# Optimization experiments

Measured on AMD Instinct MI355X. Metric: run time of the kernel, lower is better.

Reference implementation:

```python
import jax, jax.numpy as jnp
import numpy as np

TEMPERATURE = 0.2

def setup_inputs() -> dict:
    key = jax.random.key(0)
    k1, k2 = jax.random.split(key)
    projected = jax.random.normal(k1, (2048, 2, 256), dtype=jnp.float32)
    predicted = jax.random.normal(k2, (2048, 4, 256), dtype=jnp.float32)
    return {"projected": projected, "predicted": predicted}

def _l2norm(x, eps=1e-12):
    n = jnp.linalg.norm(x, axis=-1, keepdims=True)
    return x / jnp.maximum(n, eps)

def reference(projected, predicted):
    # projected: [B, Vg, D], predicted: [B, Vt, D], Vt >= Vg.
    # Single-process: all_gather is identity, rank=0 -> labels = arange(B).
    B, Vg, D = projected.shape
    Vt = predicted.shape[1]
    Vl = Vt - Vg
    p = _l2norm(projected)
    q = _l2norm(predicted)
    # All pairwise similarity matrices at once: [Vg, Vt, B, B]
    logits = jnp.einsum('bid,cjd->ijbc', p, q) / TEMPERATURE
    lse = jax.nn.logsumexpr if False else jax.scipy.special.logsumexp(logits, axis=-1)  # [Vg, Vt, B]
    diag = jnp.diagonal(logits, axis1=-2, axis2=-1)                                    # [Vg, Vt, B]
    L = jnp.mean(lse - diag, axis=-1)  # per-pair CE loss, shape [Vg, Vt]
    # global terms: i != ii, both in [0, Vg)
    global_sum = jnp.sum(L[:, :Vg] * (1.0 - jnp.eye(Vg, dtype=L.dtype)))
    num_global_terms = Vg * (Vg - 1)
    global_loss = global_sum / num_global_terms if num_global_terms > 0 else jnp.float32(0.0)
    # local terms: faithful to source -> predicted columns 0..Vl-1 (not offset)
    num_local_terms = Vg * Vl
    local_sum = jnp.sum(L[:, :Vl]) if Vl > 0 else jnp.float32(0.0)
    local_loss = local_sum / num_local_terms if num_local_terms > 0 else jnp.float32(0.0)
    num_terms = num_global_terms + num_local_terms
    total = (global_sum + local_sum) / num_terms
    return (total, global_loss, local_loss)
```

## Files before the change

kernel.cpp:

```cpp
#include <hip/hip_runtime.h>
#include <hip/hip_bf16.h>
#include <hip/hip_fp8.h>
#include <stdint.h>

#define TB 2048
#define TD 256

typedef long long                                         fp8x8;
typedef __attribute__((ext_vector_type(8)))  int          int8v;
typedef __attribute__((ext_vector_type(16))) float        f32x16;

union frag32 { fp8x8 g[4]; int8v v; };

#define SQRT5 2.23606797749979f
#define SCALE1 0x7F

__global__ __launch_bounds__(256) void nnclr_prep(const float* __restrict__ proj,
                                                  const float* __restrict__ pred,
                                                  unsigned char* __restrict__ pq2) {
    const int grp = blockIdx.x;
    const int v   = blockIdx.y;
    const int t   = threadIdx.x;

    __shared__ float rowbuf[32][260];
    __shared__ float scales[32];

    #pragma unroll
    for (int it = 0; it < 8; ++it) {
        const int f = it * 256 + t;
        const int m = f >> 6, q = f & 63;
        const int b = grp * 32 + m;
        const float4* src = (v < 2) ? (const float4*)(proj + ((size_t)b * 2 + v) * TD)
                                    : (const float4*)(pred + ((size_t)b * 4 + (v - 2)) * TD);
        const float4 val = src[q];
        *(float4*)&rowbuf[m][q * 4] = val;
    }
    __syncthreads();

    {
        const int row = t >> 3, l8 = t & 7;
        float ss = 0.f;
        #pragma unroll
        for (int n = 0; n < 32; ++n) { const float y = rowbuf[row][l8 + 8 * n]; ss += y * y; }
        ss += __shfl_xor(ss, 1, 64);
        ss += __shfl_xor(ss, 2, 64);
        ss += __shfl_xor(ss, 4, 64);
        if (l8 == 0) scales[row] = SQRT5 / fmaxf(sqrtf(ss), 1e-12f);
    }
    __syncthreads();

    unsigned int* dst32 = (unsigned int*)(pq2 + (size_t)(v * 64 + grp) * 8192);
    #pragma unroll
    for (int it = 0; it < 8; ++it) {
        const int u   = it * 256 + t;
        const int m   = u >> 6;
        const int col = (u >> 1) & 31;
        const int e4  = u & 1;
        const float sc = scales[col];
        unsigned int w = 0;
        #pragma unroll
        for (int i = 0; i < 4; ++i) {
            const float y = rowbuf[col][m * 8 + 4 * e4 + i] * sc;
            const __hip_fp8_e4m3 f8(y);
            w |= ((unsigned int)f8.__x) << (8 * i);
        }
        dst32[u] = w;
    }
}

__global__ __launch_bounds__(256, 2) void nnclr_main(const unsigned char* __restrict__ pq2,
                                                     float* __restrict__ sPart,
                                                     float* __restrict__ dPart)
{
    const int rb = blockIdx.x, ch = blockIdx.y, j = blockIdx.z;
    const int tid = threadIdx.x, lane = tid & 63, wave = tid >> 6;
    const int cl = lane & 31, hk = lane >> 5;
    const int b0 = rb * 32;

    const fp8x8* P = (const fp8x8*)pq2;
    frag32 aF0[4], aF1[4];
    #pragma unroll
    for (int kb = 0; kb < 4; ++kb) {
        #pragma unroll
        for (int q = 0; q < 4; ++q) {
            const int g = 8 * kb + 4 * hk + q;
            aF0[kb].g[q] = P[((0 * 64 + rb) * 32 + g) * 32 + cl];
            aF1[kb].g[q] = P[((1 * 64 + rb) * 32 + g) * 32 + cl];
        }
    }

    float sAcc0[16], sAcc1[16];
    #pragma unroll
    for (int r = 0; r < 16; ++r) { sAcc0[r] = 0.f; sAcc1[r] = 0.f; }
    float d0 = 0.f, d1 = 0.f;
    const int  rDiag    = (cl & 3) + 4 * (cl >> 3);
    const bool laneDiag = (((cl >> 2) & 1) == hk);

    const fp8x8* Bbase = P + (size_t)(2 + j) * 64 * 32 * 32;
    const int cg0 = ch * 16 + wave * 4;

    frag32 bf[2][4];
    #pragma unroll
    for (int kb = 0; kb < 4; ++kb)
        #pragma unroll
        for (int q = 0; q < 4; ++q)
            bf[0][kb].g[q] = Bbase[((size_t)cg0 * 32 + 8 * kb + 4 * hk + q) * 32 + cl];

    #pragma unroll
    for (int cgl = 0; cgl < 4; ++cgl) {
        const int cg = cg0 + cgl;
        if (cgl < 3) {
            #pragma unroll
            for (int kb = 0; kb < 4; ++kb)
                #pragma unroll
                for (int q = 0; q < 4; ++q)
                    bf[(cgl + 1) & 1][kb].g[q] =
                        Bbase[((size_t)(cg + 1) * 32 + 8 * kb + 4 * hk + q) * 32 + cl];
        }
        f32x16 acc0, acc1;
        #pragma unroll
        for (int r = 0; r < 16; ++r) { acc0[r] = 0.f; acc1[r] = 0.f; }
        #pragma unroll
        for (int kb = 0; kb < 4; ++kb) {
            acc0 = __builtin_amdgcn_mfma_scale_f32_32x32x64_f8f6f4(
                       aF0[kb].v, bf[cgl & 1][kb].v, acc0, 0, 0, 0, SCALE1, 0, SCALE1);
            acc1 = __builtin_amdgcn_mfma_scale_f32_32x32x64_f8f6f4(
                       aF1[kb].v, bf[cgl & 1][kb].v, acc1, 0, 0, 0, SCALE1, 0, SCALE1);
        }
        const bool diagCG = (cg == rb);
        #pragma unroll
        for (int r = 0; r < 16; ++r) {
            const float v0 = acc0[r], v1 = acc1[r];
            sAcc0[r] += __expf(v0 - 5.0f);
            sAcc1[r] += __expf(v1 - 5.0f);
            if (diagCG) {
                const bool m = laneDiag && (r == rDiag);
                d0 += m ? v0 : 0.f;
                d1 += m ? v1 : 0.f;
            }
        }
    }

    #pragma unroll
    for (int r = 0; r < 16; ++r) {
        float s0 = sAcc0[r], s1 = sAcc1[r];
        #pragma unroll
        for (int msk = 1; msk < 32; msk <<= 1) {
            s0 += __shfl_xor(s0, msk, 64);
            s1 += __shfl_xor(s1, msk, 64);
        }
        sAcc0[r] = s0; sAcc1[r] = s1;
    }

    __shared__ float sArr[2][4][32];
    __shared__ float dArr[2][4][32];
    if (cl == 0) {
        #pragma unroll
        for (int r = 0; r < 16; ++r) {
            const int rowl = (r & 3) + 8 * (r >> 2) + 4 * hk;
            sArr[0][wave][rowl] = sAcc0[r];
            sArr[1][wave][rowl] = sAcc1[r];
        }
    }
    if (laneDiag) { dArr[0][wave][cl] = d0; dArr[1][wave][cl] = d1; }
    __syncthreads();
    if (tid < 64) {
        const int i = tid >> 5, row = tid & 31;
        float s = 0.f, d = 0.f;
        #pragma unroll
        for (int w = 0; w < 4; ++w) { s += sArr[i][w][row]; d += dArr[i][w][row]; }
        const int pair = i * 2 + j;
        const int b = b0 + row;
        sPart[((size_t)pair * TB + b) * 4 + ch] = s;
        dPart[((size_t)pair * TB + b) * 4 + ch] = d;
    }
}

__global__ __launch_bounds__(1024) void nnclr_final(const float* __restrict__ sPart,
                                                    const float* __restrict__ dPart,
                                                    float* __restrict__ out) {
    const int tid = threadIdx.x;
    float acc[4] = {0.f, 0.f, 0.f, 0.f};
    #pragma unroll
    for (int k = 0; k < 8; ++k) {
        const int item = k * 1024 + tid;
        const float4 sv = ((const float4*)sPart)[item];
        const float4 dv = ((const float4*)dPart)[item];
        const float s = (sv.x + sv.y) + (sv.z + sv.w);
        const float d = (dv.x + dv.y) + (dv.z + dv.w);
        acc[k >> 1] += 5.0f + logf(s) - d;
    }
    __shared__ float red[16][4];
    const int lane = tid & 63, wave = tid >> 6;
    #pragma unroll
    for (int p = 0; p < 4; ++p) {
        #pragma unroll
        for (int m = 1; m < 64; m <<= 1) acc[p] += __shfl_xor(acc[p], m, 64);
    }
    if (lane == 0) {
        #pragma unroll
        for (int p = 0; p < 4; ++p) red[wave][p] = acc[p];
    }
    __syncthreads();
    if (tid == 0) {
        float L[4];
        #pragma unroll
        for (int p = 0; p < 4; ++p) {
            float a = 0.f;
            for (int w = 0; w < 16; ++w) a += red[w][p];
            L[p] = a / (float)TB;
        }
        const float gs = L[1] + L[2];
        const float ls = L[0] + L[1] + L[2] + L[3];
        out[0] = (gs + ls) / 6.0f;
        out[1] = gs * 0.5f;
        out[2] = ls * 0.25f;
    }
}

extern "C" void kernel_launch(void* const* d_in, const int* in_sizes, int n_in,
                              void* d_out, int out_size, void* d_ws, size_t ws_size,
                              hipStream_t stream) {
    const float* projected = (const float*)d_in[0];
    const float* predicted = (const float*)d_in[1];

    unsigned char* pq2 = (unsigned char*)d_ws;
    float* sPart = (float*)((char*)d_ws + 4u * 1024u * 1024u);
    float* dPart = sPart + (size_t)4 * TB * 4;
    float* out = (float*)d_out;

    dim3 gprep(64, 4);
    nnclr_prep<<<gprep, 256, 0, stream>>>(projected, predicted, pq2);
    dim3 gmain(64, 4, 2);
    nnclr_main<<<gmain, 256, 0, stream>>>(pq2, sPart, dPart);
    nnclr_final<<<1, 1024, 0, stream>>>(sPart, dPart, out);
}
```

Before: 26.45 us.

## Fuse prep, main and final kernels into one persistent kernel with atomic grid barrier

Merges the normalize/quantize, FP8 MFMA logsumexp, and final reduction kernels into a single 512-block launch. Blocks synchronize through a global atomic counter (spin-wait with sleep), and block 0 performs the final reduction after all partials land. The prep work is re-split so each block handles 16 rows. This removes two kernel launch gaps but adds a memset launch and a software grid barrier. That barrier relies on all 512 blocks being co-resident and adds spin latency.

```diff
diff --git a/kernel.cpp b/kernel.cpp
--- a/kernel.cpp
+++ b/kernel.cpp
@@ -15,206 +15,221 @@
 #define SQRT5 2.23606797749979f
 #define SCALE1 0x7F
 
-__global__ __launch_bounds__(256) void nnclr_prep(const float* __restrict__ proj,
-                                                  const float* __restrict__ pred,
-                                                  unsigned char* __restrict__ pq2) {
-    const int grp = blockIdx.x;
-    const int v   = blockIdx.y;
+__global__ __launch_bounds__(256, 2) void nnclr_fused(const float* __restrict__ proj,
+                                                      const float* __restrict__ pred,
+                                                      unsigned char* __restrict__ pq2,
+                                                      float* __restrict__ sPart,
+                                                      float* __restrict__ dPart,
+                                                      unsigned int* __restrict__ cnt,
+                                                      float* __restrict__ out) {
+    const int bid = blockIdx.x;
     const int t   = threadIdx.x;
 
-    __shared__ float rowbuf[32][260];
-    __shared__ float scales[32];
-
-    #pragma unroll
-    for (int it = 0; it < 8; ++it) {
-        const int f = it * 256 + t;
-        const int m = f >> 6, q = f & 63;
-        const int b = grp * 32 + m;
-        const float4* src = (v < 2) ? (const float4*)(proj + ((size_t)b * 2 + v) * TD)
-                                    : (const float4*)(pred + ((size_t)b * 4 + (v - 2)) * TD);
-        const float4 val = src[q];
-        *(float4*)&rowbuf[m][q * 4] = val;
-    }
-    __syncthreads();
+    __shared__ __align__(16) unsigned char ldsraw[16704];
+    float (*rowbuf)[260] = (float(*)[260])ldsraw;
+    float* scales = (float*)(ldsraw + 16640);
 
     {
-        const int row = t >> 3, l8 = t & 7;
-        float ss = 0.f;
-        #pragma unroll
-        for (int n = 0; n < 32; ++n) { const float y = rowbuf[row][l8 + 8 * n]; ss += y * y; }
-        ss += __shfl_xor(ss, 1, 64);
-        ss += __shfl_xor(ss, 2, 64);
-        ss += __shfl_xor(ss, 4, 64);
-        if (l8 == 0) scales[row] = SQRT5 / fmaxf(sqrtf(ss), 1e-12f);
-    }
-    __syncthreads();
-
-    unsigned int* dst32 = (unsigned int*)(pq2 + (size_t)(v * 64 + grp) * 8192);
-    #pragma unroll
-    for (int it = 0; it < 8; ++it) {
-        const int u   = it * 256 + t;
-        const int m   = u >> 6;
-        const int col = (u >> 1) & 31;
-        const int e4  = u & 1;
-        const float sc = scales[col];
-        unsigned int w = 0;
-        #pragma unroll
-        for (int i = 0; i < 4; ++i) {
-            const float y = rowbuf[col][m * 8 + 4 * e4 + i] * sc;
-            const __hip_fp8_e4m3 f8(y);
-            w |= ((unsigned int)f8.__x) << (8 * i);
-        }
-        dst32[u] = w;
-    }
-}
-
-__global__ __launch_bounds__(256, 2) void nnclr_main(const unsigned char* __restrict__ pq2,
-                                                     float* __restrict__ sPart,
-                                                     float* __restrict__ dPart)
-{
-    const int rb = blockIdx.x, ch = blockIdx.y, j = blockIdx.z;
-    const int tid = threadIdx.x, lane = tid & 63, wave = tid >> 6;
-    const int cl = lane & 31, hk = lane >> 5;
-    const int b0 = rb * 32;
-
-    const fp8x8* P = (const fp8x8*)pq2;
-    frag32 aF0[4], aF1[4];
-    #pragma unroll
-    for (int kb = 0; kb < 4; ++kb) {
-        #pragma unroll
-        for (int q = 0; q < 4; ++q) {
-            const int g = 8 * kb + 4 * hk + q;
-            aF0[kb].g[q] = P[((0 * 64 + rb) * 32 + g) * 32 + cl];
-            aF1[kb].g[q] = P[((1 * 64 + rb) * 32 + g) * 32 + cl];
-        }
-    }
-
-    float sAcc0[16], sAcc1[16];
-    #pragma unroll
-    for (int r = 0; r < 16; ++r) { sAcc0[r] = 0.f; sAcc1[r] = 0.f; }
-    float d0 = 0.f, d1 = 0.f;
-    const int  rDiag    = (cl & 3) + 4 * (cl >> 3);
-    const bool laneDiag = (((cl >> 2) & 1) == hk);
-
-    const fp8x8* Bbase = P + (size_t)(2 + j) * 64 * 32 * 32;
-    const int cg0 = ch * 16 + wave * 4;
-
-    frag32 bf[2][4];
-    #pragma unroll
-    for (int kb = 0; kb < 4; ++kb)
-        #pragma unroll
-        for (int q = 0; q < 4; ++q)
-            bf[0][kb].g[q] = Bbase[((size_t)cg0 * 32 + 8 * kb + 4 * hk + q) * 32 + cl];
-
-    #pragma unroll
-    for (int cgl = 0; cgl < 4; ++cgl) {
-        const int cg = cg0 + cgl;
-        if (cgl < 3) {
-            #pragma unroll
-            for (int kb = 0; kb < 4; ++kb)
+        const int grp = bid >> 3, v = (bid >> 1) & 3, half = bid & 1;
+        #pragma unroll
+        for (int it = 0; it < 4; ++it) {
+            const int f = it * 256 + t;
+            const int m = f >> 6, q = f & 63;
+            const int b = grp * 32 + half * 16 + m;
+            const float4* src = (v < 2) ? (const float4*)(proj + ((size_t)b * 2 + v) * TD)
+                                        : (const float4*)(pred + ((size_t)b * 4 + (v - 2)) * TD);
+            *(float4*)&rowbuf[m][q * 4] = src[q];
+        }
+        __syncthreads();
+        {
+            const int row = t >> 4, l16 = t & 15;
+            float ss = 0.f;
+            #pragma unroll
+            for (int n = 0; n < 16; ++n) { const float y = rowbuf[row][l16 + 16 * n]; ss += y * y; }
+            ss += __shfl_xor(ss, 1, 64);
+            ss += __shfl_xor(ss, 2, 64);
+            ss += __shfl_xor(ss, 4, 64);
+            ss += __shfl_xor(ss, 8, 64);
+            if (l16 == 0) scales[row] = SQRT5 / fmaxf(sqrtf(ss), 1e-12f);
+        }
+        __syncthreads();
+        unsigned int* dst32 = (unsigned int*)(pq2 + (size_t)(v * 64 + grp) * 8192);
+        #pragma unroll
+        for (int it = 0; it < 4; ++it) {
+            const int idx = it * 256 + t;
+            const int g = idx >> 5, colloc = (idx >> 1) & 15, e4 = idx & 1;
+            const float sc = scales[colloc];
+            unsigned int w = 0;
+            #pragma unroll
+            for (int i = 0; i < 4; ++i) {
+                const float y = rowbuf[colloc][g * 8 + 4 * e4 + i] * sc;
+                const __hip_fp8_e4m3 f8(y);
+                w |= ((unsigned int)f8.__x) << (8 * i);
+            }
+            dst32[g * 64 + (half * 16 + colloc) * 2 + e4] = w;
+        }
+    }
+
+    __syncthreads();
+    if (t == 0) {
+        __threadfence();
+        atomicAdd(cnt, 1u);
+        while (atomicAdd(cnt, 0u) < 512u) __builtin_amdgcn_s_sleep(16);
+        __threadfence();
+    }
+    __syncthreads();
+
+    {
+        const int rb = bid >> 3, ch = (bid >> 1) & 3, j = bid & 1;
+        const int lane = t & 63, wave = t >> 6;
+        const int cl = lane & 31, hk = lane >> 5;
+        const int b0 = rb * 32;
+
+        const fp8x8* P = (const fp8x8*)pq2;
+        frag32 aF0[4], aF1[4];
+        #pragma unroll
+        for (int kb = 0; kb < 4; ++kb) {
+            #pragma unroll
+            for (int q = 0; q < 4; ++q) {
+                const int g = 8 * kb + 4 * hk + q;
+                aF0[kb].g[q] = P[((0 * 64 + rb) * 32 + g) * 32 + cl];
+                aF1[kb].g[q] = P[((1 * 64 + rb) * 32 + g) * 32 + cl];
+            }
+        }
+
+        float sAcc0[16], sAcc1[16];
+        #pragma unroll
+        for (int r = 0; r < 16; ++r) { sAcc0[r] = 0.f; sAcc1[r] = 0.f; }
+        float d0 = 0.f, d1 = 0.f;
+        const int  rDiag    = (cl & 3) + 4 * (cl >> 3);
+        const bool laneDiag = (((cl >> 2) & 1) == hk);
+
+        const fp8x8* Bbase = P + (size_t)(2 + j) * 64 * 32 * 32;
+        const int cg0 = ch * 16 + wave * 4;
+
+        frag32 bf[2][4];
+        #pragma unroll
+        for (int kb = 0; kb < 4; ++kb)
+            #pragma unroll
+            for (int q = 0; q < 4; ++q)
+                bf[0][kb].g[q] = Bbase[((size_t)cg0 * 32 + 8 * kb + 4 * hk + q) * 32 + cl];
+
+        #pragma unroll
+        for (int cgl = 0; cgl < 4; ++cgl) {
+            const int cg = cg0 + cgl;
+            if (cgl < 3) {
                 #pragma unroll
-                for (int q = 0; q < 4; ++q)
-                    bf[(cgl + 1) & 1][kb].g[q] =
-                        Bbase[((size_t)(cg + 1) * 32 + 8 * kb + 4 * hk + q) * 32 + cl];
-        }
-        f32x16 acc0, acc1;
-        #pragma unroll
-        for (int r = 0; r < 16; ++r) { acc0[r] = 0.f; acc1[r] = 0.f; }
-        #pragma unroll
-        for (int kb = 0; kb < 4; ++kb) {
-            acc0 = __builtin_amdgcn_mfma_scale_f32_32x32x64_f8f6f4(
-                       aF0[kb].v, bf[cgl & 1][kb].v, acc0, 0, 0, 0, SCALE1, 0, SCALE1);
-            acc1 = __builtin_amdgcn_mfma_scale_f32_32x32x64_f8f6f4(
-                       aF1[kb].v, bf[cgl & 1][kb].v, acc1, 0, 0, 0, SCALE1, 0, SCALE1);
-        }
-        const bool diagCG = (cg == rb);
+                for (int kb = 0; kb < 4; ++kb)
+                    #pragma unroll
+                    for (int q = 0; q < 4; ++q)
+                        bf[(cgl + 1) & 1][kb].g[q] =
+                            Bbase[((size_t)(cg + 1) * 32 + 8 * kb + 4 * hk + q) * 32 + cl];
+            }
+            f32x16 acc0, acc1;
+            #pragma unroll
+            for (int r = 0; r < 16; ++r) { acc0[r] = 0.f; acc1[r] = 0.f; }
+            #pragma unroll
+            for (int kb = 0; kb < 4; ++kb) {
+                acc0 = __builtin_amdgcn_mfma_scale_f32_32x32x64_f8f6f4(
+                           aF0[kb].v, bf[cgl & 1][kb].v, acc0, 0, 0, 0, SCALE1, 0, SCALE1);
+                acc1 = __builtin_amdgcn_mfma_scale_f32_32x32x64_f8f6f4(
+                           aF1[kb].v, bf[cgl & 1][kb].v, acc1, 0, 0, 0, SCALE1, 0, SCALE1);
+            }
+            const bool diagCG = (cg == rb);
+            #pragma unroll
+            for (int r = 0; r < 16; ++r) {
+                const float v0 = acc0[r], v1 = acc1[r];
+                sAcc0[r] += __expf(v0 - 5.0f);
+                sAcc1[r] += __expf(v1 - 5.0f);
+                if (diagCG) {
+                    const bool m = laneDiag && (r == rDiag);
+                    d0 += m ? v0 : 0.f;
+                    d1 += m ? v1 : 0.f;
+                }
+            }
+        }
+
         #pragma unroll
         for (int r = 0; r < 16; ++r) {
-            const float v0 = acc0[r], v1 = acc1[r];
-            sAcc0[r] += __expf(v0 - 5.0f);
-            sAcc1[r] += __expf(v1 - 5.0f);
-            if (diagCG) {
-                const bool m = laneDiag && (r == rDiag);
-                d0 += m ? v0 : 0.f;
-                d1 += m ? v1 : 0.f;
-            }
-        }
-    }
-
-    #pragma unroll
-    for (int r = 0; r < 16; ++r) {
-        float s0 = sAcc0[r], s1 = sAcc1[r];
-        #pragma unroll
-        for (int msk = 1; msk < 32; msk <<= 1) {
-            s0 += __shfl_xor(s0, msk, 64);
-            s1 += __shfl_xor(s1, msk, 64);
-        }
-        sAcc0[r] = s0; sAcc1[r] = s1;
-    }
-
-    __shared__ float sArr[2][4][32];
-    __shared__ float dArr[2][4][32];
-    if (cl == 0) {
-        #pragma unroll
-        for (int r = 0; r < 16; ++r) {
-            const int rowl = (r & 3) + 8 * (r >> 2) + 4 * hk;
-            sArr[0][wave][rowl] = sAcc0[r];
-            sArr[1][wave][rowl] = sAcc1[r];
-        }
-    }
-    if (laneDiag) { dArr[0][wave][cl] = d0; dArr[1][wave][cl] = d1; }
-    __syncthreads();
-    if (tid < 64) {
-        const int i = tid >> 5, row = tid & 31;
-        float s = 0.f, d = 0.f;
-        #pragma unroll
-        for (int w = 0; w < 4; ++w) { s += sArr[i][w][row]; d += dArr[i][w][row]; }
-        const int pair = i * 2 + j;
-        const int b = b0 + row;
-        sPart[((size_t)pair * TB + b) * 4 + ch] = s;
-        dPart[((size_t)pair * TB + b) * 4 + ch] = d;
-    }
-}
-
-__global__ __launch_bounds__(1024) void nnclr_final(const float* __restrict__ sPart,
-                                                    const float* __restrict__ dPart,
-                                                    float* __restrict__ out) {
-    const int tid = threadIdx.x;
-    float acc[4] = {0.f, 0.f, 0.f, 0.f};
-    #pragma unroll
-    for (int k = 0; k < 8; ++k) {
-        const int item = k * 1024 + tid;
-        const float4 sv = ((const float4*)sPart)[item];
-        const float4 dv = ((const float4*)dPart)[item];
-        const float s = (sv.x + sv.y) + (sv.z + sv.w);
-        const float d = (dv.x + dv.y) + (dv.z + dv.w);
-        acc[k >> 1] += 5.0f + logf(s) - d;
-    }
-    __shared__ float red[16][4];
-    const int lane = tid & 63, wave = tid >> 6;
-    #pragma unroll
-    for (int p = 0; p < 4; ++p) {
-        #pragma unroll
-        for (int m = 1; m < 64; m <<= 1) acc[p] += __shfl_xor(acc[p], m, 64);
-    }
-    if (lane == 0) {
-        #pragma unroll
-        for (int p = 0; p < 4; ++p) red[wave][p] = acc[p];
-    }
-    __syncthreads();
-    if (tid == 0) {
-        float L[4];
+            float s0 = sAcc0[r], s1 = sAcc1[r];
+            #pragma unroll
+            for (int msk = 1; msk < 32; msk <<= 1) {
+                s0 += __shfl_xor(s0, msk, 64);
+                s1 += __shfl_xor(s1, msk, 64);
+            }
+            sAcc0[r] = s0; sAcc1[r] = s1;
+        }
+
+        float* sArr = (float*)ldsraw;
+        float* dArr = (float*)(ldsraw + 1024);
+        if (cl == 0) {
+            #pragma unroll
+            for (int r = 0; r < 16; ++r) {
+                const int rowl = (r & 3) + 8 * (r >> 2) + 4 * hk;
+                sArr[(0 * 4 + wave) * 32 + rowl] = sAcc0[r];
+                sArr[(1 * 4 + wave) * 32 + rowl] = sAcc1[r];
+            }
+        }
+        if (laneDiag) { dArr[(0 * 4 + wave) * 32 + cl] = d0; dArr[(1 * 4 + wave) * 32 + cl] = d1; }
+        __syncthreads();
+        if (t < 64) {
+            const int i = t >> 5, row = t & 31;
+            float s = 0.f, d = 0.f;
+            #pragma unroll
+            for (int w = 0; w < 4; ++w) {
+                s += sArr[(i * 4 + w) * 32 + row];
+                d += dArr[(i * 4 + w) * 32 + row];
+            }
+            const int pair = i * 2 + j;
+            const int b = b0 + row;
+            sPart[((size_t)pair * TB + b) * 4 + ch] = s;
+            dPart[((size_t)pair * TB + b) * 4 + ch] = d;
+        }
+    }
+
+    __syncthreads();
+    if (t == 0) { __threadfence(); atomicAdd(cnt, 1u); }
+    if (bid != 0) return;
+    if (t == 0) {
+        while (atomicAdd(cnt, 0u) < 1024u) __builtin_amdgcn_s_sleep(16);
+        __threadfence();
+    }
+    __syncthreads();
+
+    {
+        float acc[4] = {0.f, 0.f, 0.f, 0.f};
+        #pragma unroll
+        for (int k = 0; k < 32; ++k) {
+            const int item = k * 256 + t;
+            const float4 sv = ((const float4*)sPart)[item];
+            const float4 dv = ((const float4*)dPart)[item];
+            const float s = (sv.x + sv.y) + (sv.z + sv.w);
+            const float d = (dv.x + dv.y) + (dv.z + dv.w);
+            acc[k >> 3] += 5.0f + logf(s) - d;
+        }
+        float* red = (float*)ldsraw;
+        const int lane = t & 63, wave = t >> 6;
         #pragma unroll
         for (int p = 0; p < 4; ++p) {
-            float a = 0.f;
-            for (int w = 0; w < 16; ++w) a += red[w][p];
-            L[p] = a / (float)TB;
-        }
-        const float gs = L[1] + L[2];
-        const float ls = L[0] + L[1] + L[2] + L[3];
-        out[0] = (gs + ls) / 6.0f;
-        out[1] = gs * 0.5f;
-        out[2] = ls * 0.25f;
+            #pragma unroll
+            for (int m = 1; m < 64; m <<= 1) acc[p] += __shfl_xor(acc[p], m, 64);
+        }
+        if (lane == 0) {
+            #pragma unroll
+            for (int p = 0; p < 4; ++p) red[wave * 4 + p] = acc[p];
+        }
+        __syncthreads();
+        if (t == 0) {
+            float L[4];
+            #pragma unroll
+            for (int p = 0; p < 4; ++p)
+                L[p] = (red[0 * 4 + p] + red[1 * 4 + p] + red[2 * 4 + p] + red[3 * 4 + p]) / (float)TB;
+            const float gs = L[1] + L[2];
+            const float ls = L[0] + L[1] + L[2] + L[3];
+            out[0] = (gs + ls) / 6.0f;
+            out[1] = gs * 0.5f;
+            out[2] = ls * 0.25f;
+        }
     }
 }
 
@@ -227,11 +242,9 @@
     unsigned char* pq2 = (unsigned char*)d_ws;
     float* sPart = (float*)((char*)d_ws + 4u * 1024u * 1024u);
     float* dPart = sPart + (size_t)4 * TB * 4;
+    unsigned int* cnt = (unsigned int*)((char*)d_ws + 4u * 1024u * 1024u + 256u * 1024u);
     float* out = (float*)d_out;
 
-    dim3 gprep(64, 4);
-    nnclr_prep<<<gprep, 256, 0, stream>>>(projected, predicted, pq2);
-    dim3 gmain(64, 4, 2);
-    nnclr_main<<<gmain, 256, 0, stream>>>(pq2, sPart, dPart);
-    nnclr_final<<<1, 1024, 0, stream>>>(sPart, dPart, out);
+    hipMemsetAsync(cnt, 0, 4, stream);
+    nnclr_fused<<<512, 256, 0, stream>>>(projected, predicted, pq2, sPart, dPart, cnt, out);
 }
```

Result: slower. 82.60 us (+212.3%).
